# Optimization experiments

Measured on AMD Instinct MI355X. Metric: run time of the kernel, lower is better.

The kernel has to match this reference:

```python
import jax, jax.numpy as jnp
import numpy as np
import math

B, S, E, H = 4, 2048, 1024, 16

def setup_inputs() -> dict:
    key = jax.random.key(0)
    k1, k2, k3 = jax.random.split(key, 3)
    scale_in = 1.0 / math.sqrt(E)
    x = jax.random.normal(k1, (B, S, E), dtype=jnp.float32)
    W_attn = jax.random.normal(k2, (E, 3 * E), dtype=jnp.float32) * scale_in
    b_attn = jnp.zeros((3 * E,), dtype=jnp.float32)
    W_proj = jax.random.normal(k3, (E, E), dtype=jnp.float32) * scale_in
    b_proj = jnp.zeros((E,), dtype=jnp.float32)
    return {"x": x, "W_attn": W_attn, "b_attn": b_attn, "W_proj": W_proj, "b_proj": b_proj}

def reference(x, W_attn, b_attn, W_proj, b_proj):
    batch, seq, emb = x.shape
    hd = emb // H  # head_dim
    qkv = x @ W_attn + b_attn                      # [B,S,3E]
    q, k, v = jnp.split(qkv, 3, axis=-1)
    # [B,S,E] -> [B,H,S,hd]
    q = q.reshape(batch, seq, H, hd).transpose(0, 2, 1, 3)
    k = k.reshape(batch, seq, H, hd).transpose(0, 2, 1, 3)
    v = v.reshape(batch, seq, H, hd).transpose(0, 2, 1, 3)
    scores = jnp.einsum('bhqd,bhkd->bhqk', q, k) * (1.0 / math.sqrt(hd))
    causal = jnp.tril(jnp.ones((seq, seq), dtype=bool))
    scores = jnp.where(causal[None, None, :, :], scores, jnp.finfo(scores.dtype).min)
    attn = jax.nn.softmax(scores, axis=-1)         # dropout p=0 -> identity
    out = jnp.einsum('bhqk,bhkd->bhqd', attn, v)   # [B,H,S,hd]
    out = out.transpose(0, 2, 1, 3).reshape(batch, seq, emb)
    return out @ W_proj + b_proj
```

## Files before the change

kernel.cpp:

```cpp
#include <hip/hip_runtime.h>

typedef __bf16 bf16;
typedef __bf16 bf16x8_t __attribute__((ext_vector_type(8)));
typedef __bf16 bf16x4_t __attribute__((ext_vector_type(4)));
typedef float f32x4_t __attribute__((ext_vector_type(4)));

#define S_ 2048
#define E_ 1024
#define HD 64
#define LOG2E 1.4426950408889634f
#define QSCALE (0.125f * LOG2E)

__device__ __forceinline__ void gl_lds16(const bf16* g, bf16* l) {
  __builtin_amdgcn_global_load_lds(
      (const __attribute__((address_space(1))) unsigned int*)g,
      (__attribute__((address_space(3))) unsigned int*)l, 16, 0, 0);
}

__device__ __forceinline__ f32x4_t vmax4(f32x4_t a, f32x4_t b) {
  f32x4_t r;
  r[0] = fmaxf(a[0], b[0]); r[1] = fmaxf(a[1], b[1]);
  r[2] = fmaxf(a[2], b[2]); r[3] = fmaxf(a[3], b[3]);
  return r;
}

__device__ __forceinline__ void transpose_tile(const float* __restrict__ in,
                                               bf16* __restrict__ out,
                                               int R, int C, int bx, int by,
                                               float tile[32][33]) {
  int c0 = bx * 32, r0 = by * 32;
  int tx = threadIdx.x & 31, ty = threadIdx.x >> 5;
#pragma unroll
  for (int i = 0; i < 32; i += 8)
    tile[ty + i][tx] = in[(size_t)(r0 + ty + i) * C + c0 + tx];
  __syncthreads();
#pragma unroll
  for (int i = 0; i < 32; i += 8)
    out[(size_t)(c0 + ty + i) * R + r0 + tx] = (bf16)tile[tx][ty + i];
}

__global__ void prep(const float* __restrict__ x, bf16* __restrict__ xb,
                     const float* __restrict__ Wa, bf16* __restrict__ Wat,
                     const float* __restrict__ Wp, bf16* __restrict__ Wpt) {
  __shared__ float tile[32][33];
  int bid = blockIdx.x;
  if (bid < 8192) {
    int i = (bid * 256 + threadIdx.x) * 4;
    float4 v = *(const float4*)(x + i);
    bf16x4_t o = { (bf16)v.x, (bf16)v.y, (bf16)v.z, (bf16)v.w };
    *(bf16x4_t*)(xb + i) = o;
  } else if (bid < 8192 + 3072) {
    int f = bid - 8192;
    transpose_tile(Wa, Wat, 1024, 3072, f % 96, f / 96, tile);
  } else {
    int f = bid - 11264;
    transpose_tile(Wp, Wpt, 1024, 1024, f % 32, f / 32, tile);
  }
}

template <int MODE>
__global__ __launch_bounds__(256, 2)
void gemm128(const bf16* __restrict__ A, const bf16* __restrict__ Bt,
             const float* __restrict__ bias,
             bf16* __restrict__ Q, bf16* __restrict__ K, bf16* __restrict__ Vt,
             float* __restrict__ Out) {
  __shared__ __align__(16) bf16 As[128 * 64];
  __shared__ __align__(16) bf16 Bs[128 * 64];
  const int tid = threadIdx.x;
  const int wave = tid >> 6, lane = tid & 63;
  const int quad = lane >> 4, l16 = lane & 15;
  const int wm = wave >> 1, wn = wave & 1;
  const int bm = blockIdx.x, bn = blockIdx.y;

  f32x4_t acc[4][4];
#pragma unroll
  for (int i = 0; i < 4; i++)
#pragma unroll
    for (int j = 0; j < 4; j++) acc[i][j] = (f32x4_t){0.f, 0.f, 0.f, 0.f};

  for (int k0 = 0; k0 < 1024; k0 += 64) {
    __syncthreads();
#pragma unroll
    for (int it = 0; it < 4; it++) {
      int id = it * 256 + tid;
      int row = id >> 3, c = id & 7;
      int sc = (c ^ (row & 7)) * 8;
      gl_lds16(A + (size_t)(bm * 128 + row) * 1024 + k0 + sc, As + id * 8);
      gl_lds16(Bt + (size_t)(bn * 128 + row) * 1024 + k0 + sc, Bs + id * 8);
    }
    __syncthreads();
#pragma unroll
    for (int ks = 0; ks < 2; ks++) {
      bf16x8_t af[4], bfr[4];
#pragma unroll
      for (int i = 0; i < 4; i++) {
        int row = wm * 64 + i * 16 + l16;
        af[i] = *(const bf16x8_t*)&As[row * 64 + (((ks * 4 + quad) ^ (row & 7)) * 8)];
      }
#pragma unroll
      for (int j = 0; j < 4; j++) {
        int row = wn * 64 + j * 16 + l16;
        bfr[j] = *(const bf16x8_t*)&Bs[row * 64 + (((ks * 4 + quad) ^ (row & 7)) * 8)];
      }
#pragma unroll
      for (int i = 0; i < 4; i++)
#pragma unroll
        for (int j = 0; j < 4; j++)
          acc[i][j] = __builtin_amdgcn_mfma_f32_16x16x32_bf16(af[i], bfr[j], acc[i][j], 0, 0, 0);
    }
  }

  if (MODE == 0) {
#pragma unroll
    for (int j = 0; j < 4; j++) {
      int n_g = bn * 128 + wn * 64 + j * 16 + l16;
      float bv = bias[n_g];
      int which = n_g >> 10;
      int cc = n_g & 1023;
      int hh = cc >> 6, dd = cc & 63;
#pragma unroll
      for (int i = 0; i < 4; i++) {
        int m0 = bm * 128 + wm * 64 + i * 16 + quad * 4;
        int bb = m0 >> 11, ss0 = m0 & 2047;
        int bhn = bb * 16 + hh;
        if (which == 2) {
          bf16x4_t pk;
#pragma unroll
          for (int r = 0; r < 4; r++) pk[r] = (bf16)(acc[i][j][r] + bv);
          *(bf16x4_t*)&Vt[((size_t)bhn * 64 + dd) * 2048 + ss0] = pk;
        } else {
          bf16* dst = (which == 0) ? Q : K;
          float scl = (which == 0) ? QSCALE : 1.f;
#pragma unroll
          for (int r = 0; r < 4; r++)
            dst[((size_t)bhn * 2048 + ss0 + r) * 64 + dd] = (bf16)((acc[i][j][r] + bv) * scl);
        }
      }
    }
  } else {
#pragma unroll
    for (int j = 0; j < 4; j++) {
      int n_g = bn * 128 + wn * 64 + j * 16 + l16;
      float bv = bias[n_g];
#pragma unroll
      for (int i = 0; i < 4; i++) {
        int m0 = bm * 128 + wm * 64 + i * 16 + quad * 4;
#pragma unroll
        for (int r = 0; r < 4; r++)
          Out[(size_t)(m0 + r) * 1024 + n_g] = acc[i][j][r] + bv;
      }
    }
  }
}

__global__ __launch_bounds__(256, 2)
void attn_kernel(const bf16* __restrict__ Q, const bf16* __restrict__ K,
                 const bf16* __restrict__ Vt, bf16* __restrict__ O) {
  extern __shared__ __align__(16) bf16 smem[];
  bf16* Ks = smem;
  bf16* Vs = smem + 8192;
  const int tid = threadIdx.x;
  const int wave = tid >> 6, lane = tid & 63;
  const int quad = lane >> 4, l16 = lane & 15;
  const int qb = blockIdx.x, bh = blockIdx.y;
  const int b = bh >> 4, h = bh & 15;

  const bf16* Qg = Q + (size_t)bh * S_ * HD;
  const bf16* Kg = K + (size_t)bh * S_ * HD;
  const bf16* Vg = Vt + (size_t)bh * HD * S_;

  auto stage = [&](int c, int kb) {
    const bf16* Ksrc = Kg + (size_t)kb * 64 * HD;
    const bf16* Vsrc = Vg + kb * 64;
    bf16* Kd = Ks + c * 4096;
    bf16* Vd = Vs + c * 4096;
#pragma unroll
    for (int it = 0; it < 2; it++) {
      int id = it * 256 + tid;
      int row = id >> 3, cc = id & 7;
      gl_lds16(Ksrc + row * 64 + ((cc ^ (row & 7)) * 8), Kd + id * 8);
      gl_lds16(Vsrc + (size_t)row * S_ + ((cc ^ (row & 7)) * 8), Vd + id * 8);
    }
  };

  bf16x8_t qf[2][2];
#pragma unroll
  for (int ni = 0; ni < 2; ni++)
#pragma unroll
    for (int ks = 0; ks < 2; ks++)
      qf[ni][ks] = *(const bf16x8_t*)(Qg +
          (size_t)(qb * 128 + wave * 32 + ni * 16 + l16) * HD + ks * 32 + quad * 8);

  f32x4_t o[4][2];
#pragma unroll
  for (int mi = 0; mi < 4; mi++)
#pragma unroll
    for (int ni = 0; ni < 2; ni++) o[mi][ni] = (f32x4_t){0.f, 0.f, 0.f, 0.f};
  float m_[2] = {-1e30f, -1e30f}, l_[2] = {0.f, 0.f};

  const int kend = 2 * qb + 2;
  int cur = 0;
  stage(0, 0);
  __syncthreads();

  for (int kb = 0; kb < kend; kb++) {
    if (kb + 1 < kend) stage(cur ^ 1, kb + 1);

    const bf16* Kc = Ks + cur * 4096;
    const bf16* Vc = Vs + cur * 4096;

    f32x4_t sacc[4][2];
#pragma unroll
    for (int mi = 0; mi < 4; mi++)
#pragma unroll
      for (int ni = 0; ni < 2; ni++) sacc[mi][ni] = (f32x4_t){0.f, 0.f, 0.f, 0.f};
#pragma unroll
    for (int ks = 0; ks < 2; ks++)
#pragma unroll
      for (int mi = 0; mi < 4; mi++) {
        int kr = mi * 16 + l16;
        bf16x8_t kf = *(const bf16x8_t*)&Kc[kr * 64 + (((ks * 4 + quad) ^ (kr & 7)) * 8)];
        sacc[mi][0] = __builtin_amdgcn_mfma_f32_16x16x32_bf16(kf, qf[0][ks], sacc[mi][0], 0, 0, 0);
        sacc[mi][1] = __builtin_amdgcn_mfma_f32_16x16x32_bf16(kf, qf[1][ks], sacc[mi][1], 0, 0, 0);
      }

    if (kb >= 2 * qb) {
#pragma unroll
      for (int mi = 0; mi < 4; mi++)
#pragma unroll
        for (int ni = 0; ni < 2; ni++) {
          int qrow = wave * 32 + ni * 16 + l16;
          int krow = (kb - 2 * qb) * 64 + mi * 16 + quad * 4;
#pragma unroll
          for (int r = 0; r < 4; r++)
            if (krow + r > qrow) sacc[mi][ni][r] = -1e30f;
        }
    }

#pragma unroll
    for (int ni = 0; ni < 2; ni++) {
      f32x4_t t0 = vmax4(vmax4(sacc[0][ni], sacc[1][ni]),
                         vmax4(sacc[2][ni], sacc[3][ni]));
      float mx = fmaxf(fmaxf(t0[0], t0[1]), fmaxf(t0[2], t0[3]));
      mx = fmaxf(mx, __shfl_xor(mx, 16));
      mx = fmaxf(mx, __shfl_xor(mx, 32));
      float mnew = fmaxf(m_[ni], mx);
      float alpha = __builtin_amdgcn_exp2f(m_[ni] - mnew);
      m_[ni] = mnew;
      f32x4_t a0 = {0.f, 0.f, 0.f, 0.f}, a1 = {0.f, 0.f, 0.f, 0.f};
#pragma unroll
      for (int mi = 0; mi < 2; mi++) {
#pragma unroll
        for (int r = 0; r < 4; r++) {
          sacc[mi][ni][r] = __builtin_amdgcn_exp2f(sacc[mi][ni][r] - mnew);
          sacc[mi + 2][ni][r] = __builtin_amdgcn_exp2f(sacc[mi + 2][ni][r] - mnew);
        }
        a0 += sacc[mi][ni];
        a1 += sacc[mi + 2][ni];
      }
      a0 += a1;
      float rs = (a0[0] + a0[1]) + (a0[2] + a0[3]);
      rs += __shfl_xor(rs, 16);
      rs += __shfl_xor(rs, 32);
      l_[ni] = alpha * l_[ni] + rs;
#pragma unroll
      for (int mi = 0; mi < 4; mi++)
#pragma unroll
        for (int r = 0; r < 4; r++) o[mi][ni][r] *= alpha;
    }

#pragma unroll
    for (int f = 0; f < 2; f++) {
      bf16x8_t pb[2];
#pragma unroll
      for (int ni = 0; ni < 2; ni++)
#pragma unroll
        for (int r = 0; r < 4; r++) {
          pb[ni][r]     = (bf16)sacc[2 * f][ni][r];
          pb[ni][r + 4] = (bf16)sacc[2 * f + 1][ni][r];
        }
#pragma unroll
      for (int mi = 0; mi < 4; mi++) {
        int d = mi * 16 + l16;
        int e = d & 7;
        int g1 = 4 * f + (quad >> 1);
        const bf16* rp = Vc + d * 64 + (quad & 1) * 4;
        bf16x4_t lo = *(const bf16x4_t*)(rp + ((g1 ^ e) * 8));
        bf16x4_t hi = *(const bf16x4_t*)(rp + (((g1 + 2) ^ e) * 8));
        bf16x8_t vb = __builtin_shufflevector(lo, hi, 0, 1, 2, 3, 4, 5, 6, 7);
#pragma unroll
        for (int ni = 0; ni < 2; ni++)
          o[mi][ni] = __builtin_amdgcn_mfma_f32_16x16x32_bf16(vb, pb[ni], o[mi][ni], 0, 0, 0);
      }
    }

    __syncthreads();
    cur ^= 1;
  }

#pragma unroll
  for (int ni = 0; ni < 2; ni++) {
    float inv = 1.0f / l_[ni];
    int q_g = qb * 128 + wave * 32 + ni * 16 + l16;
    size_t rowb = (size_t)(b * S_ + q_g) * E_ + h * HD;
#pragma unroll
    for (int mi = 0; mi < 4; mi++) {
      bf16x4_t ov;
#pragma unroll
      for (int r = 0; r < 4; r++) ov[r] = (bf16)(o[mi][ni][r] * inv);
      *(bf16x4_t*)&O[rowb + mi * 16 + quad * 4] = ov;
    }
  }
}

extern "C" void kernel_launch(void* const* d_in, const int* in_sizes, int n_in,
                              void* d_out, int out_size, void* d_ws, size_t ws_size,
                              hipStream_t stream) {
  const float* x      = (const float*)d_in[0];
  const float* W_attn = (const float*)d_in[1];
  const float* b_attn = (const float*)d_in[2];
  const float* W_proj = (const float*)d_in[3];
  const float* b_proj = (const float*)d_in[4];
  float* out = (float*)d_out;

  bf16* xb  = (bf16*)d_ws;
  bf16* Wat = xb + 8388608ull;
  bf16* Wpt = Wat + 3145728ull;
  bf16* Qb  = Wpt + 1048576ull;
  bf16* Kb  = Qb + 8388608ull;
  bf16* Vtb = Kb + 8388608ull;
  bf16* AOb = xb;

  prep<<<12288, 256, 0, stream>>>(x, xb, W_attn, Wat, W_proj, Wpt);
  gemm128<0><<<dim3(64, 24), 256, 0, stream>>>(xb, Wat, b_attn, Qb, Kb, Vtb, nullptr);
  attn_kernel<<<dim3(16, 64), 256, 32768, stream>>>(Qb, Kb, Vtb, AOb);
  gemm128<1><<<dim3(64, 8), 256, 0, stream>>>(AOb, Wpt, b_proj, nullptr, nullptr, nullptr, out);
}
```

Baseline: 286.0 us.

## Pair causal query tiles per block for balanced attention work

Each attention block now processes two 64-row query tiles (pid and 31-pid) sequentially instead of one 128-row tile, giving every block the same number of key blocks under the causal mask. This targets load imbalance and tail effects across the grid, and also reduces diagonal masking waste. In exchange each wave covers 16 query rows instead of 32, halving reuse of K/V fragments read from LDS per MFMA. The K/V prefetch for the second tile is overlapped with the end of the first.

```diff
diff --git a/kernel.cpp b/kernel.cpp
--- a/kernel.cpp
+++ b/kernel.cpp
@@ -162,7 +162,7 @@
   const int tid = threadIdx.x;
   const int wave = tid >> 6, lane = tid & 63;
   const int quad = lane >> 4, l16 = lane & 15;
-  const int qb = blockIdx.x, bh = blockIdx.y;
+  const int pid = blockIdx.x, bh = blockIdx.y;
   const int b = bh >> 4, h = bh & 15;
 
   const bf16* Qg = Q + (size_t)bh * S_ * HD;
@@ -183,132 +183,121 @@
     }
   };
 
-  bf16x8_t qf[2][2];
-#pragma unroll
-  for (int ni = 0; ni < 2; ni++)
-#pragma unroll
-    for (int ks = 0; ks < 2; ks++)
-      qf[ni][ks] = *(const bf16x8_t*)(Qg +
-          (size_t)(qb * 128 + wave * 32 + ni * 16 + l16) * HD + ks * 32 + quad * 8);
-
-  f32x4_t o[4][2];
-#pragma unroll
-  for (int mi = 0; mi < 4; mi++)
-#pragma unroll
-    for (int ni = 0; ni < 2; ni++) o[mi][ni] = (f32x4_t){0.f, 0.f, 0.f, 0.f};
-  float m_[2] = {-1e30f, -1e30f}, l_[2] = {0.f, 0.f};
-
-  const int kend = 2 * qb + 2;
   int cur = 0;
   stage(0, 0);
-  __syncthreads();
-
-  for (int kb = 0; kb < kend; kb++) {
-    if (kb + 1 < kend) stage(cur ^ 1, kb + 1);
-
-    const bf16* Kc = Ks + cur * 4096;
-    const bf16* Vc = Vs + cur * 4096;
-
-    f32x4_t sacc[4][2];
-#pragma unroll
-    for (int mi = 0; mi < 4; mi++)
-#pragma unroll
-      for (int ni = 0; ni < 2; ni++) sacc[mi][ni] = (f32x4_t){0.f, 0.f, 0.f, 0.f};
+
+  for (int qi = 0; qi < 2; qi++) {
+    const int qp = qi ? (31 - pid) : pid;
+    bf16x8_t qf[2];
 #pragma unroll
     for (int ks = 0; ks < 2; ks++)
+      qf[ks] = *(const bf16x8_t*)(Qg +
+          (size_t)(qp * 64 + wave * 16 + l16) * HD + ks * 32 + quad * 8);
+
+    f32x4_t o[4];
+#pragma unroll
+    for (int mi = 0; mi < 4; mi++) o[mi] = (f32x4_t){0.f, 0.f, 0.f, 0.f};
+    float m_ = -1e30f, l_ = 0.f;
+
+    if (qi == 0) __syncthreads();
+
+    const int kend = qp + 1;
+    for (int kb = 0; kb < kend; kb++) {
+      if (kb + 1 < kend) stage(cur ^ 1, kb + 1);
+      else if (qi == 0) stage(cur ^ 1, 0);
+
+      const bf16* Kc = Ks + cur * 4096;
+      const bf16* Vc = Vs + cur * 4096;
+
+      f32x4_t sacc[4];
+#pragma unroll
+      for (int mi = 0; mi < 4; mi++) sacc[mi] = (f32x4_t){0.f, 0.f, 0.f, 0.f};
+#pragma unroll
+      for (int ks = 0; ks < 2; ks++)
+#pragma unroll
+        for (int mi = 0; mi < 4; mi++) {
+          int kr = mi * 16 + l16;
+          bf16x8_t kf = *(const bf16x8_t*)&Kc[kr * 64 + (((ks * 4 + quad) ^ (kr & 7)) * 8)];
+          sacc[mi] = __builtin_amdgcn_mfma_f32_16x16x32_bf16(kf, qf[ks], sacc[mi], 0, 0, 0);
+        }
+
+      if (kb == qp) {
+        int qrow = wave * 16 + l16;
+#pragma unroll
+        for (int mi = 0; mi < 4; mi++) {
+          int krow = mi * 16 + quad * 4;
+#pragma unroll
+          for (int r = 0; r < 4; r++)
+            if (krow + r > qrow) sacc[mi][r] = -1e30f;
+        }
+      }
+
+      {
+        f32x4_t t0 = vmax4(vmax4(sacc[0], sacc[1]), vmax4(sacc[2], sacc[3]));
+        float mx = fmaxf(fmaxf(t0[0], t0[1]), fmaxf(t0[2], t0[3]));
+        mx = fmaxf(mx, __shfl_xor(mx, 16));
+        mx = fmaxf(mx, __shfl_xor(mx, 32));
+        float mnew = fmaxf(m_, mx);
+        float alpha = __builtin_amdgcn_exp2f(m_ - mnew);
+        m_ = mnew;
+        f32x4_t a0 = {0.f, 0.f, 0.f, 0.f}, a1 = {0.f, 0.f, 0.f, 0.f};
+#pragma unroll
+        for (int mi = 0; mi < 2; mi++) {
+#pragma unroll
+          for (int r = 0; r < 4; r++) {
+            sacc[mi][r] = __builtin_amdgcn_exp2f(sacc[mi][r] - mnew);
+            sacc[mi + 2][r] = __builtin_amdgcn_exp2f(sacc[mi + 2][r] - mnew);
+          }
+          a0 += sacc[mi];
+          a1 += sacc[mi + 2];
+        }
+        a0 += a1;
+        float rs = (a0[0] + a0[1]) + (a0[2] + a0[3]);
+        rs += __shfl_xor(rs, 16);
+        rs += __shfl_xor(rs, 32);
+        l_ = alpha * l_ + rs;
+#pragma unroll
+        for (int mi = 0; mi < 4; mi++)
+#pragma unroll
+          for (int r = 0; r < 4; r++) o[mi][r] *= alpha;
+      }
+
+#pragma unroll
+      for (int f = 0; f < 2; f++) {
+        bf16x8_t pb;
+#pragma unroll
+        for (int r = 0; r < 4; r++) {
+          pb[r]     = (bf16)sacc[2 * f][r];
+          pb[r + 4] = (bf16)sacc[2 * f + 1][r];
+        }
+#pragma unroll
+        for (int mi = 0; mi < 4; mi++) {
+          int d = mi * 16 + l16;
+          int e = d & 7;
+          int g1 = 4 * f + (quad >> 1);
+          const bf16* rp = Vc + d * 64 + (quad & 1) * 4;
+          bf16x4_t lo = *(const bf16x4_t*)(rp + ((g1 ^ e) * 8));
+          bf16x4_t hi = *(const bf16x4_t*)(rp + (((g1 + 2) ^ e) * 8));
+          bf16x8_t vb = __builtin_shufflevector(lo, hi, 0, 1, 2, 3, 4, 5, 6, 7);
+          o[mi] = __builtin_amdgcn_mfma_f32_16x16x32_bf16(vb, pb, o[mi], 0, 0, 0);
+        }
+      }
+
+      __syncthreads();
+      cur ^= 1;
+    }
+
+    {
+      float inv = 1.0f / l_;
+      int q_g = qp * 64 + wave * 16 + l16;
+      size_t rowb = (size_t)(b * S_ + q_g) * E_ + h * HD;
 #pragma unroll
       for (int mi = 0; mi < 4; mi++) {
-        int kr = mi * 16 + l16;
-        bf16x8_t kf = *(const bf16x8_t*)&Kc[kr * 64 + (((ks * 4 + quad) ^ (kr & 7)) * 8)];
-        sacc[mi][0] = __builtin_amdgcn_mfma_f32_16x16x32_bf16(kf, qf[0][ks], sacc[mi][0], 0, 0, 0);
-        sacc[mi][1] = __builtin_amdgcn_mfma_f32_16x16x32_bf16(kf, qf[1][ks], sacc[mi][1], 0, 0, 0);
-      }
-
-    if (kb >= 2 * qb) {
-#pragma unroll
-      for (int mi = 0; mi < 4; mi++)
-#pragma unroll
-        for (int ni = 0; ni < 2; ni++) {
-          int qrow = wave * 32 + ni * 16 + l16;
-          int krow = (kb - 2 * qb) * 64 + mi * 16 + quad * 4;
-#pragma unroll
-          for (int r = 0; r < 4; r++)
-            if (krow + r > qrow) sacc[mi][ni][r] = -1e30f;
-        }
-    }
-
-#pragma unroll
-    for (int ni = 0; ni < 2; ni++) {
-      f32x4_t t0 = vmax4(vmax4(sacc[0][ni], sacc[1][ni]),
-                         vmax4(sacc[2][ni], sacc[3][ni]));
-      float mx = fmaxf(fmaxf(t0[0], t0[1]), fmaxf(t0[2], t0[3]));
-      mx = fmaxf(mx, __shfl_xor(mx, 16));
-      mx = fmaxf(mx, __shfl_xor(mx, 32));
-      float mnew = fmaxf(m_[ni], mx);
-      float alpha = __builtin_amdgcn_exp2f(m_[ni] - mnew);
-      m_[ni] = mnew;
-      f32x4_t a0 = {0.f, 0.f, 0.f, 0.f}, a1 = {0.f, 0.f, 0.f, 0.f};
-#pragma unroll
-      for (int mi = 0; mi < 2; mi++) {
-#pragma unroll
-        for (int r = 0; r < 4; r++) {
-          sacc[mi][ni][r] = __builtin_amdgcn_exp2f(sacc[mi][ni][r] - mnew);
-          sacc[mi + 2][ni][r] = __builtin_amdgcn_exp2f(sacc[mi + 2][ni][r] - mnew);
-        }
-        a0 += sacc[mi][ni];
-        a1 += sacc[mi + 2][ni];
-      }
-      a0 += a1;
-      float rs = (a0[0] + a0[1]) + (a0[2] + a0[3]);
-      rs += __shfl_xor(rs, 16);
-      rs += __shfl_xor(rs, 32);
-      l_[ni] = alpha * l_[ni] + rs;
-#pragma unroll
-      for (int mi = 0; mi < 4; mi++)
-#pragma unroll
-        for (int r = 0; r < 4; r++) o[mi][ni][r] *= alpha;
-    }
-
-#pragma unroll
-    for (int f = 0; f < 2; f++) {
-      bf16x8_t pb[2];
-#pragma unroll
-      for (int ni = 0; ni < 2; ni++)
-#pragma unroll
-        for (int r = 0; r < 4; r++) {
-          pb[ni][r]     = (bf16)sacc[2 * f][ni][r];
-          pb[ni][r + 4] = (bf16)sacc[2 * f + 1][ni][r];
-        }
-#pragma unroll
-      for (int mi = 0; mi < 4; mi++) {
-        int d = mi * 16 + l16;
-        int e = d & 7;
-        int g1 = 4 * f + (quad >> 1);
-        const bf16* rp = Vc + d * 64 + (quad & 1) * 4;
-        bf16x4_t lo = *(const bf16x4_t*)(rp + ((g1 ^ e) * 8));
-        bf16x4_t hi = *(const bf16x4_t*)(rp + (((g1 + 2) ^ e) * 8));
-        bf16x8_t vb = __builtin_shufflevector(lo, hi, 0, 1, 2, 3, 4, 5, 6, 7);
-#pragma unroll
-        for (int ni = 0; ni < 2; ni++)
-          o[mi][ni] = __builtin_amdgcn_mfma_f32_16x16x32_bf16(vb, pb[ni], o[mi][ni], 0, 0, 0);
-      }
-    }
-
-    __syncthreads();
-    cur ^= 1;
-  }
-
-#pragma unroll
-  for (int ni = 0; ni < 2; ni++) {
-    float inv = 1.0f / l_[ni];
-    int q_g = qb * 128 + wave * 32 + ni * 16 + l16;
-    size_t rowb = (size_t)(b * S_ + q_g) * E_ + h * HD;
-#pragma unroll
-    for (int mi = 0; mi < 4; mi++) {
-      bf16x4_t ov;
-#pragma unroll
-      for (int r = 0; r < 4; r++) ov[r] = (bf16)(o[mi][ni][r] * inv);
-      *(bf16x4_t*)&O[rowb + mi * 16 + quad * 4] = ov;
+        bf16x4_t ov;
+#pragma unroll
+        for (int r = 0; r < 4; r++) ov[r] = (bf16)(o[mi][r] * inv);
+        *(bf16x4_t*)&O[rowb + mi * 16 + quad * 4] = ov;
+      }
     }
   }
 }
```

After: 260.2 us. -9.0%, faster.
